# Optimization experiments

Measured on AMD Instinct MI355X. Metric: run time of the kernel, lower is better.

The kernel has to match this reference:

```python
import jax, jax.numpy as jnp
import numpy as np

QUERY_DIM = 1024
CONTEXT_DIM = 768
HEADS = 16
DIM_HEAD = 64
INNER = HEADS * DIM_HEAD  # 1024
SCALE = DIM_HEAD ** -0.5


def setup_inputs() -> dict:
    key = jax.random.key(0)
    ks = jax.random.split(key, 8)
    b, nq, nkv = 4, 2048, 1024
    x = jax.random.normal(ks[0], (b, nq, QUERY_DIM), dtype=jnp.float32)
    context = jax.random.normal(ks[1], (b, nkv, CONTEXT_DIM), dtype=jnp.float32)
    mask = jax.random.randint(ks[2], (b, nkv), 0, 2).astype(jnp.bool_)
    s = 0.02
    Wq = jax.random.normal(ks[3], (QUERY_DIM, INNER), dtype=jnp.float32) * s
    Wk = jax.random.normal(ks[4], (CONTEXT_DIM, INNER), dtype=jnp.float32) * s
    Wv = jax.random.normal(ks[5], (CONTEXT_DIM, INNER), dtype=jnp.float32) * s
    Wo = jax.random.normal(ks[6], (INNER, QUERY_DIM), dtype=jnp.float32) * s
    bo = jnp.zeros((QUERY_DIM,), dtype=jnp.float32)
    return {"x": x, "context": context, "mask": mask,
            "Wq": Wq, "Wk": Wk, "Wv": Wv, "Wo": Wo, "bo": bo}


def reference(x, context, mask, Wq, Wk, Wv, Wo, bo):
    b, nq, _ = x.shape
    nkv = context.shape[1]
    h, d = HEADS, DIM_HEAD
    # QKV projections (no bias, as in nn.Linear(..., bias=False))
    q = (x @ Wq).reshape(b, nq, h, d).transpose(0, 2, 1, 3)       # [b,h,i,d]
    k = (context @ Wk).reshape(b, nkv, h, d).transpose(0, 2, 1, 3)  # [b,h,j,d]
    v = (context @ Wv).reshape(b, nkv, h, d).transpose(0, 2, 1, 3)  # [b,h,j,d]
    sim = jnp.einsum('bhid,bhjd->bhij', q, k) * SCALE
    # mask is per-key [b, j]; broadcast over heads and query positions
    neg = jnp.finfo(sim.dtype).min
    sim = jnp.where(mask[:, None, None, :], sim, neg)
    attn = jax.nn.softmax(sim, axis=-1)
    out = jnp.einsum('bhij,bhjd->bhid', attn, v)                  # [b,h,i,d]
    out = out.transpose(0, 2, 1, 3).reshape(b, nq, h * d)          # [b,i,hd]
    return out @ Wo + bo
```

## Files before the change

### kernel.cpp

```cpp
#include <hip/hip_runtime.h>

typedef unsigned short u16;
typedef __attribute__((ext_vector_type(8))) __bf16 bf16x8;
typedef __attribute__((ext_vector_type(4))) float f32x4;
typedef __attribute__((ext_vector_type(4))) u16 u16x4;

#define NB 4
#define NQ 2048
#define NKV 1024
#define NH 16
#define DH 64
#define DIN 1024
#define DCTX 768
#define NEGBIG -1e30f
#define QSC 0.180336881f

__device__ inline u16 f2bf(float f) {
  unsigned u = __builtin_bit_cast(unsigned, f);
  u += 0x7FFFu + ((u >> 16) & 1u);
  return (u16)(u >> 16);
}

__device__ inline unsigned cvtpk(float lo, float hi) {
  unsigned r;
  asm("v_cvt_pk_bf16_f32 %0, %1, %2" : "=v"(r) : "v"(lo), "v"(hi));
  return r;
}

__device__ inline float exp2a(float x) {
  float r;
  asm("v_exp_f32 %0, %1" : "=v"(r) : "v"(x));
  return r;
}

__global__ __launch_bounds__(256) void build_bias(const void* __restrict__ mask,
                                                  float* __restrict__ biasg) {
  __shared__ int notInt, notFloat;
  if (threadIdx.x == 0) { notInt = 0; notFloat = 0; }
  __syncthreads();
  const unsigned* mw = (const unsigned*)mask;
  int bad_i = 0, bad_f = 0;
#pragma unroll
  for (int e = 0; e < 4; e++) {
    unsigned v = mw[threadIdx.x * 4 + e];
    if (v > 1u) bad_i = 1;
    if (v != 0u && v != 0x3f800000u) bad_f = 1;
  }
  if (bad_i) atomicOr(&notInt, 1);
  if (bad_f) atomicOr(&notFloat, 1);
  __syncthreads();
  const int isInt = !notInt, isFloat = !notFloat;
  for (int i = threadIdx.x; i < NB * NKV; i += 256) {
    bool on;
    if (isInt)        on = ((const int*)mask)[i] != 0;
    else if (isFloat) on = ((const float*)mask)[i] != 0.f;
    else              on = ((const unsigned char*)mask)[i] != 0;
    biasg[i] = on ? 0.f : NEGBIG;
  }
}

__global__ __launch_bounds__(256) void cvt_bf16(const float* __restrict__ in,
                                                u16* __restrict__ out, int n) {
  int i = (blockIdx.x * 256 + threadIdx.x) * 4;
  if (i >= n) return;
  float4 v = *(const float4*)(in + i);
  u16x4 o = { f2bf(v.x), f2bf(v.y), f2bf(v.z), f2bf(v.w) };
  *(u16x4*)(out + i) = o;
}

__global__ __launch_bounds__(256) void transpose_cvt(const float* __restrict__ W,
                                                     u16* __restrict__ Wt, int K, int N) {
  __shared__ float tile[32][33];
  int n0 = blockIdx.x * 32, k0 = blockIdx.y * 32;
  int tx = threadIdx.x & 31, ty = threadIdx.x >> 5;
#pragma unroll
  for (int i = 0; i < 32; i += 8)
    tile[ty + i][tx] = W[(size_t)(k0 + ty + i) * N + n0 + tx];
  __syncthreads();
#pragma unroll
  for (int i = 0; i < 32; i += 8)
    Wt[(size_t)(n0 + ty + i) * K + k0 + tx] = f2bf(tile[tx][ty + i]);
}

template<int STORE_MODE>
__global__ __launch_bounds__(256) void gemm_bt(const u16* __restrict__ A,
                                               const u16* __restrict__ Bt,
                                               void* __restrict__ Cout,
                                               const float* __restrict__ bias,
                                               int M, int N, int K) {
  __shared__ __align__(16) u16 As[2][128 * 32];
  __shared__ __align__(16) u16 Bs[2][128 * 32];
  const int t = threadIdx.x, w = t >> 6, l = t & 63, g = l >> 4, m16 = l & 15;
  const int brow = blockIdx.y * 128, bcol = blockIdx.x * 128;
  const int wr = w >> 1, wc = w & 1;
  const int r_a = t >> 2;
  const int kb  = (t & 3) * 8;
  const int nk = K >> 5;
  f32x4 acc[4][4] = {};

#define G_STAGE(ks, bsel)                                                              \
  {                                                                                    \
    int k0_ = (ks) << 5;                                                               \
    _Pragma("unroll")                                                                  \
    for (int i = 0; i < 2; i++) {                                                      \
      const u16* ga = A + (size_t)(brow + i * 64 + r_a) * K + k0_ + kb;                \
      __builtin_amdgcn_global_load_lds(                                                \
          (const __attribute__((address_space(1))) void*)ga,                           \
          (__attribute__((address_space(3))) void*)((char*)As + (bsel) * 8192 + i * 4096 + w * 1024), \
          16, 0, 0);                                                                   \
      const u16* gb = Bt + (size_t)(bcol + i * 64 + r_a) * K + k0_ + kb;               \
      __builtin_amdgcn_global_load_lds(                                                \
          (const __attribute__((address_space(1))) void*)gb,                           \
          (__attribute__((address_space(3))) void*)((char*)Bs + (bsel) * 8192 + i * 4096 + w * 1024), \
          16, 0, 0);                                                                   \
    }                                                                                  \
  }

  G_STAGE(0, 0);
  asm volatile("s_waitcnt vmcnt(0)" ::: "memory");
  __builtin_amdgcn_s_barrier();

  for (int ks = 0; ks < nk; ++ks) {
    const int cur = ks & 1;
    bf16x8 af[4], bfr[4];
#pragma unroll
    for (int m = 0; m < 4; m++)
      af[m] = *(const bf16x8*)(&As[cur][(wr * 64 + m * 16 + m16) * 32 + g * 8]);
#pragma unroll
    for (int n = 0; n < 4; n++)
      bfr[n] = *(const bf16x8*)(&Bs[cur][(wc * 64 + n * 16 + m16) * 32 + g * 8]);
    if (ks + 1 < nk) G_STAGE(ks + 1, cur ^ 1);
#pragma unroll
    for (int m = 0; m < 4; m++)
#pragma unroll
      for (int n = 0; n < 4; n++)
        acc[m][n] = __builtin_amdgcn_mfma_f32_16x16x32_bf16(af[m], bfr[n], acc[m][n], 0, 0, 0);
    asm volatile("s_waitcnt vmcnt(0)" ::: "memory");
    __builtin_amdgcn_s_barrier();
  }
#undef G_STAGE

#pragma unroll
  for (int m = 0; m < 4; m++) {
    int grow = brow + wr * 64 + m * 16 + g * 4;
#pragma unroll
    for (int n = 0; n < 4; n++) {
      int gcol = bcol + wc * 64 + n * 16 + m16;
#pragma unroll
      for (int r = 0; r < 4; r++) {
        size_t off = (size_t)(grow + r) * N + gcol;
        if (STORE_MODE == 0)      ((float*)Cout)[off] = acc[m][n][r] + bias[gcol];
        else if (STORE_MODE == 1) ((u16*)Cout)[off] = f2bf(acc[m][n][r]);
        else                      ((u16*)Cout)[off] = f2bf(acc[m][n][r] * QSC);
      }
    }
  }
}

__global__ __launch_bounds__(256) void attn(const u16* __restrict__ Q, const u16* __restrict__ Kb,
                                            const u16* __restrict__ Vb,
                                            const float* __restrict__ biasg,
                                            u16* __restrict__ O, int kvs) {
  const int qt = blockIdx.x, h = blockIdx.y, b = blockIdx.z;
  const int t = threadIdx.x, w = t >> 6, l = t & 63, g = l >> 4, m16 = l & 15;

  __shared__ __align__(16) u16 Kl[2][64 * 64];
  __shared__ __align__(16) u16 Vt[2][64 * 64];
  __shared__ __align__(16) unsigned Pl[4][16 * 36];
  __shared__ float biasl[NKV];

  for (int i = t; i < NKV; i += 256) biasl[i] = biasg[(size_t)b * NKV + i];

  const int qrowA = qt * 128 + w * 32 + m16;
  const u16* qpA = Q + (size_t)(b * NQ + qrowA) * DIN + h * DH;
  bf16x8 qA0 = *(const bf16x8*)(qpA + g * 8);
  bf16x8 qA1 = *(const bf16x8*)(qpA + 32 + g * 8);
  const u16* qpB = qpA + 16 * DIN;
  bf16x8 qB0 = *(const bf16x8*)(qpB + g * 8);
  bf16x8 qB1 = *(const bf16x8*)(qpB + 32 + g * 8);

  f32x4 oA[4] = {}, oB[4] = {};
  float lA = 0.f, lB = 0.f;

  union VV { u16 e[16]; int4 q[2]; };
  VV vv;
  const int swv = (l ^ (l >> 3)) & 7;

#define GATHER_V(j0)                                                          \
  {                                                                           \
    const u16* gv = Vb + (size_t)(b * NKV + (j0) + w * 16) * kvs + h * DH + l; \
    _Pragma("unroll")                                                         \
    for (int e = 0; e < 16; e++) vv.e[e] = gv[(size_t)e * kvs];               \
  }
#define STAGE_K(j0, bsel)                                                     \
  {                                                                           \
    _Pragma("unroll")                                                         \
    for (int n = 0; n < 2; n++) {                                             \
      int j_ = n * 32 + (t >> 3);                                             \
      int c_ = (t & 7) ^ (j_ & 7);                                            \
      const u16* gk = Kb + (size_t)(b * NKV + (j0) + j_) * kvs + h * DH + c_ * 8; \
      __builtin_amdgcn_global_load_lds(                                       \
          (const __attribute__((address_space(1))) void*)gk,                  \
          (__attribute__((address_space(3))) void*)((char*)Kl + (bsel) * 8192 + n * 4096 + t * 16), \
          16, 0, 0);                                                          \
    }                                                                         \
  }
#define WRITE_V(bsel)                                                         \
  {                                                                           \
    _Pragma("unroll")                                                         \
    for (int kk = 0; kk < 2; kk++) {                                          \
      int cp = (2 * w + kk) ^ swv;                                            \
      *(int4*)(&Vt[bsel][l * 64 + cp * 8]) = vv.q[kk];                        \
    }                                                                         \
  }

  GATHER_V(0);
  STAGE_K(0, 0);
  asm volatile("s_waitcnt vmcnt(0)" ::: "memory");
  WRITE_V(0);
  asm volatile("s_waitcnt lgkmcnt(0)" ::: "memory");
  __builtin_amdgcn_s_barrier();

  for (int it = 0; it < 16; ++it) {
    const int cur = it & 1, nxt = cur ^ 1;
    const int j0 = it * 64;
    if (it + 1 < 16) {
      GATHER_V(j0 + 64);
      STAGE_K(j0 + 64, nxt);
    }

    f32x4 sA[4], sB[4];
#pragma unroll
    for (int jt = 0; jt < 4; jt++) {
      int jr = jt * 16 + m16;
      const u16* krow = &Kl[cur][jr * 64];
      bf16x8 kf0 = *(const bf16x8*)(krow + ((g ^ (jr & 7)) * 8));
      bf16x8 kf1 = *(const bf16x8*)(krow + (((4 + g) ^ (jr & 7)) * 8));
      f32x4 z = {};
      f32x4 t0 = __builtin_amdgcn_mfma_f32_16x16x32_bf16(kf0, qA0, z, 0, 0, 0);
      sA[jt]   = __builtin_amdgcn_mfma_f32_16x16x32_bf16(kf1, qA1, t0, 0, 0, 0);
      f32x4 t1 = __builtin_amdgcn_mfma_f32_16x16x32_bf16(kf0, qB0, z, 0, 0, 0);
      sB[jt]   = __builtin_amdgcn_mfma_f32_16x16x32_bf16(kf1, qB1, t1, 0, 0, 0);
    }
    float4 b4[4];
#pragma unroll
    for (int jt = 0; jt < 4; jt++) b4[jt] = *(const float4*)&biasl[j0 + jt * 16 + g * 4];

    unsigned* plw = &Pl[w][0];
    {
#pragma unroll
      for (int jt = 0; jt < 4; jt++) {
        float p0 = exp2a(sA[jt][0] + b4[jt].x);
        float p1 = exp2a(sA[jt][1] + b4[jt].y);
        float p2 = exp2a(sA[jt][2] + b4[jt].z);
        float p3 = exp2a(sA[jt][3] + b4[jt].w);
        lA += (p0 + p1) + (p2 + p3);
        uint2 u; u.x = cvtpk(p0, p1); u.y = cvtpk(p2, p3);
        *(uint2*)&plw[m16 * 36 + jt * 8 + 2 * g] = u;
      }
      asm volatile("" ::: "memory");
      bf16x8 pf0 = *(const bf16x8*)&plw[m16 * 36 + 4 * g];
      bf16x8 pf1 = *(const bf16x8*)&plw[m16 * 36 + 16 + 4 * g];
#pragma unroll
      for (int dt = 0; dt < 4; dt++) {
        int d = dt * 16 + m16;
        int swd = (d ^ (d >> 3)) & 7;
        const u16* vrow = &Vt[cur][d * 64];
        bf16x8 vf0 = *(const bf16x8*)(vrow + ((g ^ swd) * 8));
        bf16x8 vf1 = *(const bf16x8*)(vrow + (((4 + g) ^ swd) * 8));
        oA[dt] = __builtin_amdgcn_mfma_f32_16x16x32_bf16(pf0, vf0, oA[dt], 0, 0, 0);
        oA[dt] = __builtin_amdgcn_mfma_f32_16x16x32_bf16(pf1, vf1, oA[dt], 0, 0, 0);
      }
    }
    asm volatile("" ::: "memory");
    {
#pragma unroll
      for (int jt = 0; jt < 4; jt++) {
        float p0 = exp2a(sB[jt][0] + b4[jt].x);
        float p1 = exp2a(sB[jt][1] + b4[jt].y);
        float p2 = exp2a(sB[jt][2] + b4[jt].z);
        float p3 = exp2a(sB[jt][3] + b4[jt].w);
        lB += (p0 + p1) + (p2 + p3);
        uint2 u; u.x = cvtpk(p0, p1); u.y = cvtpk(p2, p3);
        *(uint2*)&plw[m16 * 36 + jt * 8 + 2 * g] = u;
      }
      asm volatile("" ::: "memory");
      bf16x8 pf0 = *(const bf16x8*)&plw[m16 * 36 + 4 * g];
      bf16x8 pf1 = *(const bf16x8*)&plw[m16 * 36 + 16 + 4 * g];
#pragma unroll
      for (int dt = 0; dt < 4; dt++) {
        int d = dt * 16 + m16;
        int swd = (d ^ (d >> 3)) & 7;
        const u16* vrow = &Vt[cur][d * 64];
        bf16x8 vf0 = *(const bf16x8*)(vrow + ((g ^ swd) * 8));
        bf16x8 vf1 = *(const bf16x8*)(vrow + (((4 + g) ^ swd) * 8));
        oB[dt] = __builtin_amdgcn_mfma_f32_16x16x32_bf16(pf0, vf0, oB[dt], 0, 0, 0);
        oB[dt] = __builtin_amdgcn_mfma_f32_16x16x32_bf16(pf1, vf1, oB[dt], 0, 0, 0);
      }
    }
    asm volatile("s_waitcnt vmcnt(0)" ::: "memory");
    if (it + 1 < 16) WRITE_V(nxt);
    asm volatile("s_waitcnt lgkmcnt(0)" ::: "memory");
    __builtin_amdgcn_s_barrier();
  }
#undef GATHER_V
#undef STAGE_K
#undef WRITE_V

  lA += __shfl_xor(lA, 16); lA += __shfl_xor(lA, 32);
  lB += __shfl_xor(lB, 16); lB += __shfl_xor(lB, 32);
  float invA[4], invB[4];
#pragma unroll
  for (int r = 0; r < 4; r++) {
    invA[r] = 1.f / __shfl(lA, g * 4 + r);
    invB[r] = 1.f / __shfl(lB, g * 4 + r);
  }
  u16* opA = O + (size_t)(b * NQ + qt * 128 + w * 32) * DIN + h * DH;
  u16* opB = opA + 16 * DIN;
#pragma unroll
  for (int dt = 0; dt < 4; dt++)
#pragma unroll
    for (int r = 0; r < 4; r++) {
      opA[(size_t)(g * 4 + r) * DIN + dt * 16 + m16] = f2bf(oA[dt][r] * invA[r]);
      opB[(size_t)(g * 4 + r) * DIN + dt * 16 + m16] = f2bf(oB[dt][r] * invB[r]);
    }
}

extern "C" void kernel_launch(void* const* d_in, const int* in_sizes, int n_in,
                              void* d_out, int out_size, void* d_ws, size_t ws_size,
                              hipStream_t stream) {
  const float* x   = (const float*)d_in[0];
  const float* ctx = (const float*)d_in[1];
  const void*  mask = (const void*)d_in[2];
  const float* Wq  = (const float*)d_in[3];
  const float* Wk  = (const float*)d_in[4];
  const float* Wv  = (const float*)d_in[5];
  const float* Wo  = (const float*)d_in[6];
  const float* bo  = (const float*)d_in[7];
  float* out = (float*)d_out;

  char* ws = (char*)d_ws;
  u16* xb   = (u16*)(ws);
  u16* cb   = (u16*)(ws + 16777216);
  u16* wqt  = (u16*)(ws + 23068672);
  u16* wkv  = (u16*)(ws + 25165824);
  u16* wot  = (u16*)(ws + 28311552);
  u16* qb   = (u16*)(ws + 30408704);
  u16* kvb  = (u16*)(ws + 47185920);
  float* biasg = (float*)(ws + 63963136);
  u16* ab   = xb;

  build_bias<<<1, 256, 0, stream>>>(mask, biasg);
  cvt_bf16<<<8192, 256, 0, stream>>>(x, xb, 8388608);
  cvt_bf16<<<3072, 256, 0, stream>>>(ctx, cb, 3145728);
  transpose_cvt<<<dim3(32, 32), 256, 0, stream>>>(Wq, wqt, 1024, 1024);
  transpose_cvt<<<dim3(32, 24), 256, 0, stream>>>(Wk, wkv, 768, 1024);
  transpose_cvt<<<dim3(32, 24), 256, 0, stream>>>(Wv, wkv + 1024 * 768, 768, 1024);
  transpose_cvt<<<dim3(32, 32), 256, 0, stream>>>(Wo, wot, 1024, 1024);

  gemm_bt<2><<<dim3(8, 64), 256, 0, stream>>>(xb, wqt, qb, nullptr, 8192, 1024, 1024);
  gemm_bt<1><<<dim3(16, 32), 256, 0, stream>>>(cb, wkv, kvb, nullptr, 4096, 2048, 768);

  attn<<<dim3(16, 16, 4), 256, 0, stream>>>(qb, kvb, kvb + 1024, biasg, ab, 2048);

  gemm_bt<0><<<dim3(8, 64), 256, 0, stream>>>(ab, wot, out, bo, 8192, 1024, 1024);
}
```

Measured before the change: 275.0 us.

## Triple-buffer GEMM, merge QKV launches, pre-transpose V, halve attention tile

The GEMM kernel moves to a three-stage LDS pipeline with partial vmcnt waits, and one launch now covers both the Q and KV projections through a block-index split. A new vtrans kernel writes V transposed per head into global memory. Attention can then stage V with async global_load_lds instead of strided scalar gathers and register-to-LDS writes. Attention blocks now handle 64 query rows instead of 128, which doubles the grid, drops the second query tile per wave, and adds an extra kernel plus a round trip of V through memory.

```diff
diff --git a/kernel.cpp b/kernel.cpp
--- a/kernel.cpp
+++ b/kernel.cpp
@@ -82,16 +82,42 @@
     Wt[(size_t)(n0 + ty + i) * K + k0 + tx] = f2bf(tile[tx][ty + i]);
 }
 
-template<int STORE_MODE>
-__global__ __launch_bounds__(256) void gemm_bt(const u16* __restrict__ A,
-                                               const u16* __restrict__ Bt,
-                                               void* __restrict__ Cout,
-                                               const float* __restrict__ bias,
-                                               int M, int N, int K) {
-  __shared__ __align__(16) u16 As[2][128 * 32];
-  __shared__ __align__(16) u16 Bs[2][128 * 32];
+__global__ __launch_bounds__(256) void vtrans(const u16* __restrict__ kvb, u16* __restrict__ vtg) {
+  __shared__ __align__(16) u16 tile[64][72];
+  const int t = threadIdx.x;
+  const int jt = blockIdx.x, bh = blockIdx.y;
+  const int b = bh >> 4, h = bh & 15;
+  const int j0 = jt * 64;
+  const int jl = t >> 2, c2 = t & 3;
+  const u16* src = kvb + (size_t)(b * 1024 + j0 + jl) * 2048 + 1024 + h * 64 + c2 * 16;
+  *(int4*)&tile[jl][c2 * 16]     = *(const int4*)(src);
+  *(int4*)&tile[jl][c2 * 16 + 8] = *(const int4*)(src + 8);
+  __syncthreads();
+  const int dl = t >> 2;
+  union { u16 e[16]; int4 q[2]; } pk;
+#pragma unroll
+  for (int e = 0; e < 16; e++) pk.e[e] = tile[c2 * 16 + e][dl];
+  u16* dst = vtg + (size_t)(bh * 64 + dl) * 1024 + j0 + c2 * 16;
+  *(int4*)dst       = pk.q[0];
+  *(int4*)(dst + 8) = pk.q[1];
+}
+
+__global__ __launch_bounds__(256) void gemm_pipe(
+    const u16* __restrict__ A0, const u16* __restrict__ B0, void* __restrict__ C0,
+    const float* __restrict__ bias0, int N0, int K0, int mode0, int gx0,
+    const u16* __restrict__ A1, const u16* __restrict__ B1, void* __restrict__ C1,
+    const float* __restrict__ bias1, int N1, int K1, int mode1, int gx1, int split) {
+  __shared__ __align__(16) u16 As[3 * 4096];
+  __shared__ __align__(16) u16 Bs[3 * 4096];
+  const u16 *A, *Bt; void* Cout; const float* bias;
+  int N, K, mode, bx, by;
+  {
+    int bi = blockIdx.x;
+    if (bi < split) { A = A0; Bt = B0; Cout = C0; bias = bias0; N = N0; K = K0; mode = mode0; bx = bi % gx0; by = bi / gx0; }
+    else { bi -= split; A = A1; Bt = B1; Cout = C1; bias = bias1; N = N1; K = K1; mode = mode1; bx = bi % gx1; by = bi / gx1; }
+  }
   const int t = threadIdx.x, w = t >> 6, l = t & 63, g = l >> 4, m16 = l & 15;
-  const int brow = blockIdx.y * 128, bcol = blockIdx.x * 128;
+  const int brow = by * 128, bcol = bx * 128;
   const int wr = w >> 1, wc = w & 1;
   const int r_a = t >> 2;
   const int kb  = (t & 3) * 8;
@@ -117,26 +143,27 @@
   }
 
   G_STAGE(0, 0);
-  asm volatile("s_waitcnt vmcnt(0)" ::: "memory");
-  __builtin_amdgcn_s_barrier();
-
+  G_STAGE(1, 1);
+  int cur = 0, stg = 2;
   for (int ks = 0; ks < nk; ++ks) {
-    const int cur = ks & 1;
+    if (ks + 1 < nk) asm volatile("s_waitcnt vmcnt(4)" ::: "memory");
+    else             asm volatile("s_waitcnt vmcnt(0)" ::: "memory");
+    asm volatile("s_barrier" ::: "memory");
     bf16x8 af[4], bfr[4];
 #pragma unroll
     for (int m = 0; m < 4; m++)
-      af[m] = *(const bf16x8*)(&As[cur][(wr * 64 + m * 16 + m16) * 32 + g * 8]);
+      af[m] = *(const bf16x8*)(&As[cur * 4096 + (wr * 64 + m * 16 + m16) * 32 + g * 8]);
 #pragma unroll
     for (int n = 0; n < 4; n++)
-      bfr[n] = *(const bf16x8*)(&Bs[cur][(wc * 64 + n * 16 + m16) * 32 + g * 8]);
-    if (ks + 1 < nk) G_STAGE(ks + 1, cur ^ 1);
+      bfr[n] = *(const bf16x8*)(&Bs[cur * 4096 + (wc * 64 + n * 16 + m16) * 32 + g * 8]);
+    if (ks + 2 < nk) G_STAGE(ks + 2, stg);
 #pragma unroll
     for (int m = 0; m < 4; m++)
 #pragma unroll
       for (int n = 0; n < 4; n++)
         acc[m][n] = __builtin_amdgcn_mfma_f32_16x16x32_bf16(af[m], bfr[n], acc[m][n], 0, 0, 0);
-    asm volatile("s_waitcnt vmcnt(0)" ::: "memory");
-    __builtin_amdgcn_s_barrier();
+    cur = (cur == 2) ? 0 : cur + 1;
+    stg = (stg == 2) ? 0 : stg + 1;
   }
 #undef G_STAGE
 
@@ -149,87 +176,78 @@
 #pragma unroll
       for (int r = 0; r < 4; r++) {
         size_t off = (size_t)(grow + r) * N + gcol;
-        if (STORE_MODE == 0)      ((float*)Cout)[off] = acc[m][n][r] + bias[gcol];
-        else if (STORE_MODE == 1) ((u16*)Cout)[off] = f2bf(acc[m][n][r]);
-        else                      ((u16*)Cout)[off] = f2bf(acc[m][n][r] * QSC);
+        if (mode == 0)      ((float*)Cout)[off] = acc[m][n][r] + bias[gcol];
+        else if (mode == 1) ((u16*)Cout)[off] = f2bf(acc[m][n][r]);
+        else                ((u16*)Cout)[off] = f2bf(acc[m][n][r] * QSC);
       }
     }
   }
 }
 
 __global__ __launch_bounds__(256) void attn(const u16* __restrict__ Q, const u16* __restrict__ Kb,
-                                            const u16* __restrict__ Vb,
+                                            const u16* __restrict__ Vt_g,
                                             const float* __restrict__ biasg,
-                                            u16* __restrict__ O, int kvs) {
+                                            u16* __restrict__ O) {
   const int qt = blockIdx.x, h = blockIdx.y, b = blockIdx.z;
   const int t = threadIdx.x, w = t >> 6, l = t & 63, g = l >> 4, m16 = l & 15;
-
-  __shared__ __align__(16) u16 Kl[2][64 * 64];
-  __shared__ __align__(16) u16 Vt[2][64 * 64];
+  const int bh = b * NH + h;
+
+  __shared__ __align__(16) u16 Kl[2][4096];
+  __shared__ __align__(16) u16 Vt[2][4096];
   __shared__ __align__(16) unsigned Pl[4][16 * 36];
   __shared__ float biasl[NKV];
 
   for (int i = t; i < NKV; i += 256) biasl[i] = biasg[(size_t)b * NKV + i];
 
-  const int qrowA = qt * 128 + w * 32 + m16;
-  const u16* qpA = Q + (size_t)(b * NQ + qrowA) * DIN + h * DH;
-  bf16x8 qA0 = *(const bf16x8*)(qpA + g * 8);
-  bf16x8 qA1 = *(const bf16x8*)(qpA + 32 + g * 8);
-  const u16* qpB = qpA + 16 * DIN;
-  bf16x8 qB0 = *(const bf16x8*)(qpB + g * 8);
-  bf16x8 qB1 = *(const bf16x8*)(qpB + 32 + g * 8);
-
-  f32x4 oA[4] = {}, oB[4] = {};
-  float lA = 0.f, lB = 0.f;
-
-  union VV { u16 e[16]; int4 q[2]; };
-  VV vv;
-  const int swv = (l ^ (l >> 3)) & 7;
-
-#define GATHER_V(j0)                                                          \
-  {                                                                           \
-    const u16* gv = Vb + (size_t)(b * NKV + (j0) + w * 16) * kvs + h * DH + l; \
-    _Pragma("unroll")                                                         \
-    for (int e = 0; e < 16; e++) vv.e[e] = gv[(size_t)e * kvs];               \
-  }
+  const int qrow = qt * 64 + w * 16 + m16;
+  const u16* qp = Q + (size_t)(b * NQ + qrow) * DIN + h * DH;
+  bf16x8 qA0 = *(const bf16x8*)(qp + g * 8);
+  bf16x8 qA1 = *(const bf16x8*)(qp + 32 + g * 8);
+
+  f32x4 oA[4] = {};
+  float lA = 0.f;
+
 #define STAGE_K(j0, bsel)                                                     \
   {                                                                           \
     _Pragma("unroll")                                                         \
     for (int n = 0; n < 2; n++) {                                             \
       int j_ = n * 32 + (t >> 3);                                             \
       int c_ = (t & 7) ^ (j_ & 7);                                            \
-      const u16* gk = Kb + (size_t)(b * NKV + (j0) + j_) * kvs + h * DH + c_ * 8; \
+      const u16* gk = Kb + (size_t)(b * NKV + (j0) + j_) * 2048 + h * DH + c_ * 8; \
       __builtin_amdgcn_global_load_lds(                                       \
           (const __attribute__((address_space(1))) void*)gk,                  \
           (__attribute__((address_space(3))) void*)((char*)Kl + (bsel) * 8192 + n * 4096 + t * 16), \
           16, 0, 0);                                                          \
     }                                                                         \
   }
-#define WRITE_V(bsel)                                                         \
+#define STAGE_V(j0, bsel)                                                     \
   {                                                                           \
     _Pragma("unroll")                                                         \
-    for (int kk = 0; kk < 2; kk++) {                                          \
-      int cp = (2 * w + kk) ^ swv;                                            \
-      *(int4*)(&Vt[bsel][l * 64 + cp * 8]) = vv.q[kk];                        \
+    for (int n = 0; n < 2; n++) {                                             \
+      int d_ = n * 32 + (t >> 3);                                             \
+      int c_ = (t & 7) ^ (d_ & 7);                                            \
+      const u16* gv = Vt_g + (size_t)(bh * 64 + d_) * 1024 + (j0) + c_ * 8;   \
+      __builtin_amdgcn_global_load_lds(                                       \
+          (const __attribute__((address_space(1))) void*)gv,                  \
+          (__attribute__((address_space(3))) void*)((char*)Vt + (bsel) * 8192 + n * 4096 + t * 16), \
+          16, 0, 0);                                                          \
     }                                                                         \
   }
 
-  GATHER_V(0);
   STAGE_K(0, 0);
-  asm volatile("s_waitcnt vmcnt(0)" ::: "memory");
-  WRITE_V(0);
-  asm volatile("s_waitcnt lgkmcnt(0)" ::: "memory");
-  __builtin_amdgcn_s_barrier();
+  STAGE_V(0, 0);
+  asm volatile("s_waitcnt vmcnt(0) lgkmcnt(0)" ::: "memory");
+  asm volatile("s_barrier" ::: "memory");
 
   for (int it = 0; it < 16; ++it) {
     const int cur = it & 1, nxt = cur ^ 1;
     const int j0 = it * 64;
     if (it + 1 < 16) {
-      GATHER_V(j0 + 64);
       STAGE_K(j0 + 64, nxt);
-    }
-
-    f32x4 sA[4], sB[4];
+      STAGE_V(j0 + 64, nxt);
+    }
+
+    f32x4 sA[4];
 #pragma unroll
     for (int jt = 0; jt < 4; jt++) {
       int jr = jt * 16 + m16;
@@ -239,91 +257,50 @@
       f32x4 z = {};
       f32x4 t0 = __builtin_amdgcn_mfma_f32_16x16x32_bf16(kf0, qA0, z, 0, 0, 0);
       sA[jt]   = __builtin_amdgcn_mfma_f32_16x16x32_bf16(kf1, qA1, t0, 0, 0, 0);
-      f32x4 t1 = __builtin_amdgcn_mfma_f32_16x16x32_bf16(kf0, qB0, z, 0, 0, 0);
-      sB[jt]   = __builtin_amdgcn_mfma_f32_16x16x32_bf16(kf1, qB1, t1, 0, 0, 0);
     }
     float4 b4[4];
 #pragma unroll
     for (int jt = 0; jt < 4; jt++) b4[jt] = *(const float4*)&biasl[j0 + jt * 16 + g * 4];
 
     unsigned* plw = &Pl[w][0];
-    {
-#pragma unroll
-      for (int jt = 0; jt < 4; jt++) {
-        float p0 = exp2a(sA[jt][0] + b4[jt].x);
-        float p1 = exp2a(sA[jt][1] + b4[jt].y);
-        float p2 = exp2a(sA[jt][2] + b4[jt].z);
-        float p3 = exp2a(sA[jt][3] + b4[jt].w);
-        lA += (p0 + p1) + (p2 + p3);
-        uint2 u; u.x = cvtpk(p0, p1); u.y = cvtpk(p2, p3);
-        *(uint2*)&plw[m16 * 36 + jt * 8 + 2 * g] = u;
-      }
-      asm volatile("" ::: "memory");
-      bf16x8 pf0 = *(const bf16x8*)&plw[m16 * 36 + 4 * g];
-      bf16x8 pf1 = *(const bf16x8*)&plw[m16 * 36 + 16 + 4 * g];
-#pragma unroll
-      for (int dt = 0; dt < 4; dt++) {
-        int d = dt * 16 + m16;
-        int swd = (d ^ (d >> 3)) & 7;
-        const u16* vrow = &Vt[cur][d * 64];
-        bf16x8 vf0 = *(const bf16x8*)(vrow + ((g ^ swd) * 8));
-        bf16x8 vf1 = *(const bf16x8*)(vrow + (((4 + g) ^ swd) * 8));
-        oA[dt] = __builtin_amdgcn_mfma_f32_16x16x32_bf16(pf0, vf0, oA[dt], 0, 0, 0);
-        oA[dt] = __builtin_amdgcn_mfma_f32_16x16x32_bf16(pf1, vf1, oA[dt], 0, 0, 0);
-      }
+#pragma unroll
+    for (int jt = 0; jt < 4; jt++) {
+      float p0 = exp2a(sA[jt][0] + b4[jt].x);
+      float p1 = exp2a(sA[jt][1] + b4[jt].y);
+      float p2 = exp2a(sA[jt][2] + b4[jt].z);
+      float p3 = exp2a(sA[jt][3] + b4[jt].w);
+      lA += (p0 + p1) + (p2 + p3);
+      uint2 u; u.x = cvtpk(p0, p1); u.y = cvtpk(p2, p3);
+      *(uint2*)&plw[m16 * 36 + jt * 8 + 2 * g] = u;
     }
     asm volatile("" ::: "memory");
-    {
-#pragma unroll
-      for (int jt = 0; jt < 4; jt++) {
-        float p0 = exp2a(sB[jt][0] + b4[jt].x);
-        float p1 = exp2a(sB[jt][1] + b4[jt].y);
-        float p2 = exp2a(sB[jt][2] + b4[jt].z);
-        float p3 = exp2a(sB[jt][3] + b4[jt].w);
-        lB += (p0 + p1) + (p2 + p3);
-        uint2 u; u.x = cvtpk(p0, p1); u.y = cvtpk(p2, p3);
-        *(uint2*)&plw[m16 * 36 + jt * 8 + 2 * g] = u;
-      }
-      asm volatile("" ::: "memory");
-      bf16x8 pf0 = *(const bf16x8*)&plw[m16 * 36 + 4 * g];
-      bf16x8 pf1 = *(const bf16x8*)&plw[m16 * 36 + 16 + 4 * g];
-#pragma unroll
-      for (int dt = 0; dt < 4; dt++) {
-        int d = dt * 16 + m16;
-        int swd = (d ^ (d >> 3)) & 7;
-        const u16* vrow = &Vt[cur][d * 64];
-        bf16x8 vf0 = *(const bf16x8*)(vrow + ((g ^ swd) * 8));
-        bf16x8 vf1 = *(const bf16x8*)(vrow + (((4 + g) ^ swd) * 8));
-        oB[dt] = __builtin_amdgcn_mfma_f32_16x16x32_bf16(pf0, vf0, oB[dt], 0, 0, 0);
-        oB[dt] = __builtin_amdgcn_mfma_f32_16x16x32_bf16(pf1, vf1, oB[dt], 0, 0, 0);
-      }
+    bf16x8 pf0 = *(const bf16x8*)&plw[m16 * 36 + 4 * g];
+    bf16x8 pf1 = *(const bf16x8*)&plw[m16 * 36 + 16 + 4 * g];
+#pragma unroll
+    for (int dt = 0; dt < 4; dt++) {
+      int d = dt * 16 + m16;
+      const u16* vrow = &Vt[cur][d * 64];
+      bf16x8 vf0 = *(const bf16x8*)(vrow + ((g ^ (d & 7)) * 8));
+      bf16x8 vf1 = *(const bf16x8*)(vrow + (((4 + g) ^ (d & 7)) * 8));
+      oA[dt] = __builtin_amdgcn_mfma_f32_16x16x32_bf16(pf0, vf0, oA[dt], 0, 0, 0);
+      oA[dt] = __builtin_amdgcn_mfma_f32_16x16x32_bf16(pf1, vf1, oA[dt], 0, 0, 0);
     }
     asm volatile("s_waitcnt vmcnt(0)" ::: "memory");
-    if (it + 1 < 16) WRITE_V(nxt);
-    asm volatile("s_waitcnt lgkmcnt(0)" ::: "memory");
-    __builtin_amdgcn_s_barrier();
-  }
-#undef GATHER_V
+    asm volatile("s_barrier" ::: "memory");
+  }
 #undef STAGE_K
-#undef WRITE_V
+#undef STAGE_V
 
   lA += __shfl_xor(lA, 16); lA += __shfl_xor(lA, 32);
-  lB += __shfl_xor(lB, 16); lB += __shfl_xor(lB, 32);
-  float invA[4], invB[4];
-#pragma unroll
-  for (int r = 0; r < 4; r++) {
-    invA[r] = 1.f / __shfl(lA, g * 4 + r);
-    invB[r] = 1.f / __shfl(lB, g * 4 + r);
-  }
-  u16* opA = O + (size_t)(b * NQ + qt * 128 + w * 32) * DIN + h * DH;
-  u16* opB = opA + 16 * DIN;
+  float invA[4];
+#pragma unroll
+  for (int r = 0; r < 4; r++) invA[r] = 1.f / __shfl(lA, g * 4 + r);
+  u16* op = O + (size_t)(b * NQ + qt * 64 + w * 16) * DIN + h * DH;
 #pragma unroll
   for (int dt = 0; dt < 4; dt++)
 #pragma unroll
-    for (int r = 0; r < 4; r++) {
-      opA[(size_t)(g * 4 + r) * DIN + dt * 16 + m16] = f2bf(oA[dt][r] * invA[r]);
-      opB[(size_t)(g * 4 + r) * DIN + dt * 16 + m16] = f2bf(oB[dt][r] * invB[r]);
-    }
+    for (int r = 0; r < 4; r++)
+      op[(size_t)(g * 4 + r) * DIN + dt * 16 + m16] = f2bf(oA[dt][r] * invA[r]);
 }
 
 extern "C" void kernel_launch(void* const* d_in, const int* in_sizes, int n_in,
@@ -347,6 +324,7 @@
   u16* wot  = (u16*)(ws + 28311552);
   u16* qb   = (u16*)(ws + 30408704);
   u16* kvb  = (u16*)(ws + 47185920);
+  u16* vtg  = (u16*)(ws + 16777216);
   float* biasg = (float*)(ws + 63963136);
   u16* ab   = xb;
 
@@ -358,10 +336,15 @@
   transpose_cvt<<<dim3(32, 24), 256, 0, stream>>>(Wv, wkv + 1024 * 768, 768, 1024);
   transpose_cvt<<<dim3(32, 32), 256, 0, stream>>>(Wo, wot, 1024, 1024);
 
-  gemm_bt<2><<<dim3(8, 64), 256, 0, stream>>>(xb, wqt, qb, nullptr, 8192, 1024, 1024);
-  gemm_bt<1><<<dim3(16, 32), 256, 0, stream>>>(cb, wkv, kvb, nullptr, 4096, 2048, 768);
-
-  attn<<<dim3(16, 16, 4), 256, 0, stream>>>(qb, kvb, kvb + 1024, biasg, ab, 2048);
-
-  gemm_bt<0><<<dim3(8, 64), 256, 0, stream>>>(ab, wot, out, bo, 8192, 1024, 1024);
-}
+  gemm_pipe<<<1024, 256, 0, stream>>>(
+      xb, wqt, qb, nullptr, 1024, 1024, 2, 8,
+      cb, wkv, kvb, nullptr, 2048, 768, 1, 16, 512);
+
+  vtrans<<<dim3(16, 64), 256, 0, stream>>>(kvb, vtg);
+
+  attn<<<dim3(32, 16, 4), 256, 0, stream>>>(qb, kvb, vtg, biasg, ab);
+
+  gemm_pipe<<<512, 256, 0, stream>>>(
+      ab, wot, out, bo, 1024, 1024, 0, 8,
+      ab, wot, out, bo, 1024, 1024, 0, 8, 512);
+}
```

After: 290.0 us. 5.4% more time.
